# Kernel optimization log

Hardware: AMD Instinct MI355X
Metric: run time of the kernel (lower is better)

## Reference

```python
import jax, jax.numpy as jnp
import numpy as np

B, N, NB = 48, 512, 4096
SEG = ((0, 1600), (1600, 3200), (3200, 4096))  # static bond-type segments (C-C, C-H, H-H)
H, L = 8, 2                                     # be MLP hidden width / depth
BOTOL = 0.001
LP1, OVUN3, OVUN4, OVUN6, OVUN7, OVUN8 = 10.0, 5.0, 3.0, 6.0, 1.0, 12.0
BOX = 10.0


def _taper(r, rmin, rmax):
    # piecewise smooth step used on the uncorrected bond-order terms
    r3 = jnp.where(r > rmax, 1.0, 0.0)
    ok = (r <= rmax) & (r > rmin)
    r2 = jnp.where(ok, r, 0.0)
    r20 = jnp.where(ok, 1.0, 0.0)
    rterm = 1.0 / (rmin - rmax) ** 3
    rm = rmin * r20
    rd = rm - r2
    trm1 = rm + 2.0 * r2 - 3.0 * rmax * r20
    return rterm * rd * rd * trm1 + r3


def _div_if(y, x):
    return y / jnp.where(x != 0.0, x, 1e-8)


def setup_inputs():
    key = jax.random.key(0)
    ks = jax.random.split(key, 10)
    x = jax.random.uniform(ks[0], (B, N, 3), dtype=jnp.float32) * BOX
    cell = jnp.eye(3, dtype=jnp.float32) * BOX
    rcell = jnp.eye(3, dtype=jnp.float32) / BOX
    i = jax.random.randint(ks[1], (NB,), 0, N)
    j = jax.random.randint(ks[2], (NB,), 0, N)
    j = jnp.where(i == j, (j + 1) % N, j)
    bdid = jnp.stack([i, j], axis=1).astype(jnp.int32)
    atom_type = jax.random.randint(ks[3], (N,), 0, 2).astype(jnp.int32)
    # per-bond-type ReaxFF parameters (realistic magnitudes)
    bond_rosi = jnp.array([1.38, 1.12, 0.74], jnp.float32)
    bond_bo1 = jnp.array([-0.075, -0.05, -0.08], jnp.float32)
    bond_bo2 = jnp.array([6.8, 6.9, 6.0], jnp.float32)
    bond_ropi = jnp.array([1.28, 1.00, 0.70], jnp.float32)
    bond_bo3 = jnp.array([-0.20, -0.15, -0.20], jnp.float32)
    bond_bo4 = jnp.array([8.5, 7.0, 8.0], jnp.float32)
    bond_ropp = jnp.array([1.20, 0.90, 0.65], jnp.float32)
    bond_bo5 = jnp.array([-0.30, -0.25, -0.30], jnp.float32)
    bond_bo6 = jnp.array([10.0, 9.0, 10.0], jnp.float32)
    bond_Desi = jnp.array([145.0, 180.0, 160.0], jnp.float32)
    # per-species parameters (C, H)
    sp_val = jnp.array([4.0, 1.0], jnp.float32)
    sp_vale = jnp.array([4.0, 1.0], jnp.float32)
    sp_lp2 = jnp.array([0.1, 0.0], jnp.float32)
    sp_ovun2 = jnp.array([-5.0, -10.0], jnp.float32)
    sp_ovun5 = jnp.array([30.0, 0.0], jnp.float32)
    # fe (bond-energy) MLP weights per bond type: Wi (3,H), Wh (H,H)xL, Wo (H,1)
    fe_wi = jax.random.normal(ks[4], (3, 3, H), jnp.float32) * 0.5
    fe_w = jax.random.normal(ks[5], (3, L, H, H), jnp.float32) * 0.5
    fe_b = jax.random.normal(ks[6], (3, L, H), jnp.float32) * 0.5
    fe_wo = jax.random.normal(ks[7], (3, H, 1), jnp.float32) * 0.5
    fe_bo = jax.random.normal(ks[8], (3, 1), jnp.float32) * 0.5
    return dict(x=x, cell=cell, rcell=rcell, bdid=bdid, atom_type=atom_type,
                bond_rosi=bond_rosi, bond_bo1=bond_bo1, bond_bo2=bond_bo2,
                bond_ropi=bond_ropi, bond_bo3=bond_bo3, bond_bo4=bond_bo4,
                bond_ropp=bond_ropp, bond_bo5=bond_bo5, bond_bo6=bond_bo6,
                bond_Desi=bond_Desi, sp_val=sp_val, sp_vale=sp_vale,
                sp_lp2=sp_lp2, sp_ovun2=sp_ovun2, sp_ovun5=sp_ovun5,
                fe_wi=fe_wi, fe_w=fe_w, fe_b=fe_b, fe_wo=fe_wo, fe_bo=fe_bo)


def _forward(x, cell, rcell, bdid, atom_type,
             bond_rosi, bond_bo1, bond_bo2, bond_ropi, bond_bo3, bond_bo4,
             bond_ropp, bond_bo5, bond_bo6, bond_Desi,
             sp_val, sp_vale, sp_lp2, sp_ovun2, sp_ovun5,
             fe_wi, fe_w, fe_b, fe_wo, fe_bo):
    # --- all-pairs distances with minimum-image wrapping (fvr + rcell/cell) ---
    vr = x[:, :, None, :] - x[:, None, :, :]              # [B,N,N,3]
    vrf = vr @ rcell
    vrf = jnp.where(vrf - 0.5 > 0, vrf - 1.0, vrf)
    vrf = jnp.where(vrf + 0.5 < 0, vrf + 1.0, vrf)
    vr = vrf @ cell
    r = jnp.sqrt(jnp.sum(vr * vr, axis=3))                # [B,N,N]
    ii, jj = bdid[:, 0], bdid[:, 1]
    rbd_all = r[:, ii, jj]                                # [B,NB]

    si_l, pi_l, pp_l, ebd_l = [], [], [], []
    for t, (s0, s1) in enumerate(SEG):
        rbd = rbd_all[:, s0:s1]
        # uncorrected bond orders (get_bondorder_uc)
        eterm1 = (1.0 + BOTOL) * jnp.exp(bond_bo1[t] * (rbd / bond_rosi[t]) ** bond_bo2[t])
        eterm2 = jnp.exp(bond_bo3[t] * (rbd / bond_ropi[t]) ** bond_bo4[t])
        eterm3 = jnp.exp(bond_bo5[t] * (rbd / bond_ropp[t]) ** bond_bo6[t])
        bosi = _taper(eterm1, BOTOL, 2.0 * BOTOL) * (eterm1 - BOTOL)
        bopi = _taper(eterm2, BOTOL, 2.0 * BOTOL) * eterm2
        bopp = _taper(eterm3, BOTOL, 2.0 * BOTOL) * eterm3
        # bond-energy sigmoid MLP (fnn 'fe'): input [bosi,bopi,bopp]
        X = jnp.stack([bosi, bopi, bopp], axis=-1)        # [B,nb_t,3]
        h = jax.nn.sigmoid(jnp.einsum('bni,ih->bnh', X, fe_wi[t]))
        for l in range(L):
            h = jax.nn.sigmoid(h @ fe_w[t, l] + fe_b[t, l])
        esi = jax.nn.sigmoid(h @ fe_wo[t] + fe_bo[t])[..., 0]
        ebd_l.append(-bond_Desi[t] * esi)
        si_l.append(bosi); pi_l.append(bopi); pp_l.append(bopp)

    bosi = jnp.concatenate(si_l, axis=1)
    bopi = jnp.concatenate(pi_l, axis=1)
    bopp = jnp.concatenate(pp_l, axis=1)
    ebond = jnp.sum(jnp.concatenate(ebd_l, axis=1), axis=1)   # [B]

    # per-atom coordination via symmetric scatter of bond orders
    bo = bosi + bopi + bopp
    bpi = bopi + bopp
    zeros = jnp.zeros((x.shape[0], x.shape[1]), x.dtype)
    Delta = zeros.at[:, ii].add(bo).at[:, jj].add(bo)
    Delta_pi = zeros.at[:, ii].add(bpi).at[:, jj].add(bpi)
    SO = zeros.at[:, ii].add(bosi).at[:, jj].add(bosi)

    # species-indexed gathers of atomic params (self.s[st][sp] boolean gathers)
    val = sp_val[atom_type][None, :]
    vale = sp_vale[atom_type][None, :]
    lp2 = sp_lp2[atom_type][None, :]
    ovun2 = sp_ovun2[atom_type][None, :]
    ovun5 = sp_ovun5[atom_type][None, :]

    # --- elone ---
    Nlp = 0.5 * (vale - val)
    delta_e = 0.5 * (Delta - vale)
    De = -jax.nn.relu(-jnp.ceil(delta_e))
    nlp = -De + jnp.exp(-LP1 * 4.0 * jnp.square(1.0 + delta_e - De))
    Delta_lp = jax.nn.relu(Nlp - nlp + 1.0) - 1.0
    Elone = lp2 * Delta_lp / (1.0 + jnp.exp(-75.0 * Delta_lp))

    # --- eover ---
    delta_lpcorr = Delta - val - Delta_lp / (1.0 + OVUN3 * jnp.exp(OVUN4 * Delta_pi))
    otrm1 = _div_if(1.0, delta_lpcorr + val)
    Eover = SO * otrm1 * delta_lpcorr * jax.nn.sigmoid(-ovun2 * delta_lpcorr)

    # --- eunder ---
    expeu1 = jnp.exp(OVUN6 * delta_lpcorr)
    eu1 = jax.nn.sigmoid(ovun2 * delta_lpcorr)
    eu2 = 1.0 / (1.0 + OVUN7 * jnp.exp(OVUN8 * Delta_pi))
    Eunder = -ovun5 * (1.0 - expeu1) * eu1 * eu2

    return ebond + jnp.sum(Elone + Eover + Eunder, axis=1)   # [B]


def reference(x, cell, rcell, bdid, atom_type,
              bond_rosi, bond_bo1, bond_bo2, bond_ropi, bond_bo3, bond_bo4,
              bond_ropp, bond_bo5, bond_bo6, bond_Desi,
              sp_val, sp_vale, sp_lp2, sp_ovun2, sp_ovun5,
              fe_wi, fe_w, fe_b, fe_wo, fe_bo):
    return _forward(x, cell, rcell, bdid, atom_type,
                    bond_rosi, bond_bo1, bond_bo2, bond_ropi, bond_bo3, bond_bo4,
                    bond_ropp, bond_bo5, bond_bo6, bond_Desi,
                    sp_val, sp_vale, sp_lp2, sp_ovun2, sp_ovun5,
                    fe_wi, fe_w, fe_b, fe_wo, fe_bo)
```

## Files before the change

### kernel.cpp

```cpp
#include <hip/hip_runtime.h>
#include <math.h>

#define B_    48
#define N_    512
#define NBOND 4096
#define H_    8
#define L_    2
#define G_    16
#define TPB1  256
#define BPB   (NBOND / G_)
#define TPB2  512

#define LOG2E 1.44269504f

__device__ __forceinline__ float rcpf(float x)  { return __builtin_amdgcn_rcpf(x); }
__device__ __forceinline__ float exp2g(float x) { return __builtin_amdgcn_exp2f(x); }
__device__ __forceinline__ float log2g(float x) { return __builtin_amdgcn_logf(x); }
__device__ __forceinline__ float expg(float x)  { return exp2g(x * LOG2E); }
__device__ __forceinline__ float sigf(float x)  { return rcpf(1.0f + expg(-x)); }

__device__ __forceinline__ float taperf(float r) {
    const float rmin = 0.001f, rmax = 0.002f;
    const float d = rmin - rmax;
    const float rterm = 1.0f / (d * d * d);
    float r3  = (r > rmax) ? 1.0f : 0.0f;
    bool ok   = (r <= rmax) && (r > rmin);
    float r2  = ok ? r : 0.0f;
    float r20 = ok ? 1.0f : 0.0f;
    float rm   = rmin * r20;
    float rd   = rm - r2;
    float trm1 = rm + 2.0f * r2 - 3.0f * rmax * r20;
    return rterm * rd * rd * trm1 + r3;
}

#define WI_OFF   0
#define W_OFF    72
#define BV_OFF   456
#define WO_OFF   504
#define BO_OFF   528
#define WTOT     531

__global__ __launch_bounds__(TPB1) void bond_kernel(
    const float* __restrict__ x, const float* __restrict__ cell, const float* __restrict__ rcell,
    const int*  __restrict__ bdid,
    const float* __restrict__ rosi, const float* __restrict__ bo1, const float* __restrict__ bo2,
    const float* __restrict__ ropi, const float* __restrict__ bo3, const float* __restrict__ bo4,
    const float* __restrict__ ropp, const float* __restrict__ bo5, const float* __restrict__ bo6,
    const float* __restrict__ Desi,
    const float* __restrict__ wi, const float* __restrict__ w, const float* __restrict__ bvec,
    const float* __restrict__ wo, const float* __restrict__ bo_out,
    float* __restrict__ pPart, float* __restrict__ pEbd)
{
    const int b   = blockIdx.x / G_;
    const int g   = blockIdx.x % G_;
    const int tid = threadIdx.x;

    __shared__ float sS[N_], sP[N_];
    __shared__ float sw[WTOT];
    __shared__ float sder[30];
    __shared__ float swave[TPB1 / 64];

    #pragma unroll
    for (int q = tid; q < N_; q += TPB1) { sS[q] = 0.0f; sP[q] = 0.0f; }
    for (int q = tid; q < WTOT; q += TPB1) {
        float v;
        if      (q < W_OFF)  v = wi[q - WI_OFF];
        else if (q < BV_OFF) v = w[q - W_OFF];
        else if (q < WO_OFF) v = bvec[q - BV_OFF];
        else if (q < BO_OFF) v = wo[q - WO_OFF];
        else                 v = bo_out[q - BO_OFF];
        sw[q] = v;
    }
    if (tid < 3) {
        sder[tid * 10 + 0] = log2g(rosi[tid]);
        sder[tid * 10 + 1] = log2g(ropi[tid]);
        sder[tid * 10 + 2] = log2g(ropp[tid]);
        sder[tid * 10 + 3] = bo1[tid] * LOG2E;
        sder[tid * 10 + 4] = bo3[tid] * LOG2E;
        sder[tid * 10 + 5] = bo5[tid] * LOG2E;
        sder[tid * 10 + 6] = bo2[tid];
        sder[tid * 10 + 7] = bo4[tid];
        sder[tid * 10 + 8] = bo6[tid];
        sder[tid * 10 + 9] = Desi[tid];
    }
    float c00 = cell[0], c01 = cell[1], c02 = cell[2];
    float c10 = cell[3], c11 = cell[4], c12 = cell[5];
    float c20 = cell[6], c21 = cell[7], c22 = cell[8];
    float q00 = rcell[0], q01 = rcell[1], q02 = rcell[2];
    float q10 = rcell[3], q11 = rcell[4], q12 = rcell[5];
    float q20 = rcell[6], q21 = rcell[7], q22 = rcell[8];
    __syncthreads();

    const float* xb = x + (size_t)b * (N_ * 3);

    int k = g * BPB + tid;
    int t = (k < 1600) ? 0 : ((k < 3200) ? 1 : 2);
    const float* dc = sder + t * 10;

    int2 ij = ((const int2*)bdid)[k];
    int i = ij.x, j = ij.y;

    float vx = xb[3 * i + 0] - xb[3 * j + 0];
    float vy = xb[3 * i + 1] - xb[3 * j + 1];
    float vz = xb[3 * i + 2] - xb[3 * j + 2];

    float f0 = vx * q00 + vy * q10 + vz * q20;
    float f1 = vx * q01 + vy * q11 + vz * q21;
    float f2 = vx * q02 + vy * q12 + vz * q22;
    f0 = (f0 - 0.5f > 0.0f) ? f0 - 1.0f : f0;  f0 = (f0 + 0.5f < 0.0f) ? f0 + 1.0f : f0;
    f1 = (f1 - 0.5f > 0.0f) ? f1 - 1.0f : f1;  f1 = (f1 + 0.5f < 0.0f) ? f1 + 1.0f : f1;
    f2 = (f2 - 0.5f > 0.0f) ? f2 - 1.0f : f2;  f2 = (f2 + 0.5f < 0.0f) ? f2 + 1.0f : f2;
    float wx = f0 * c00 + f1 * c10 + f2 * c20;
    float wy = f0 * c01 + f1 * c11 + f2 * c21;
    float wz = f0 * c02 + f1 * c12 + f2 * c22;
    float r = __builtin_amdgcn_sqrtf(wx * wx + wy * wy + wz * wz);

    float lr = log2g(r);
    float p1 = exp2g(dc[6] * (lr - dc[0]));
    float p2 = exp2g(dc[7] * (lr - dc[1]));
    float p3 = exp2g(dc[8] * (lr - dc[2]));
    float e1 = 1.001f * exp2g(dc[3] * p1);
    float e2 = exp2g(dc[4] * p2);
    float e3 = exp2g(dc[5] * p3);
    float bosi = taperf(e1) * (e1 - 0.001f);
    float bopi = taperf(e2) * e2;
    float bopp = taperf(e3) * e3;

    const float* Wi = sw + WI_OFF + t * 24;
    const float* Wm = sw + W_OFF  + t * (L_ * H_ * H_);
    const float* Bv = sw + BV_OFF + t * (L_ * H_);
    const float* Wo = sw + WO_OFF + t * H_;
    float h[H_], h2[H_];
    #pragma unroll
    for (int hh = 0; hh < H_; ++hh) {
        float s = bosi * Wi[0 * H_ + hh] + bopi * Wi[1 * H_ + hh] + bopp * Wi[2 * H_ + hh];
        h[hh] = sigf(s);
    }
    #pragma unroll
    for (int l = 0; l < L_; ++l) {
        #pragma unroll
        for (int ho = 0; ho < H_; ++ho) {
            float s = Bv[l * H_ + ho];
            #pragma unroll
            for (int hi = 0; hi < H_; ++hi)
                s += h[hi] * Wm[l * (H_ * H_) + hi * H_ + ho];
            h2[ho] = sigf(s);
        }
        #pragma unroll
        for (int hh = 0; hh < H_; ++hh) h[hh] = h2[hh];
    }
    float o = sw[BO_OFF + t];
    #pragma unroll
    for (int hi = 0; hi < H_; ++hi) o += h[hi] * Wo[hi];
    float ebd = -dc[9] * sigf(o);

    float bpi = bopi + bopp;
    atomicAdd(&sS[i], bosi); atomicAdd(&sS[j], bosi);
    atomicAdd(&sP[i], bpi);  atomicAdd(&sP[j], bpi);
    __syncthreads();

    float* pd = pPart + (size_t)(b * G_ + g) * (2 * N_);
    #pragma unroll
    for (int q = tid; q < N_; q += TPB1) {
        pd[q]      = sS[q];
        pd[N_ + q] = sP[q];
    }

    float v = ebd;
    for (int off = 32; off > 0; off >>= 1) v += __shfl_down(v, off, 64);
    int lane = tid & 63, wid = tid >> 6;
    if (lane == 0) swave[wid] = v;
    __syncthreads();
    if (tid == 0) {
        float s = 0.0f;
        #pragma unroll
        for (int wv = 0; wv < TPB1 / 64; ++wv) s += swave[wv];
        pEbd[b * G_ + g] = s;
    }
}

__global__ __launch_bounds__(TPB2) void atom_kernel(
    const int* __restrict__ atype,
    const float* __restrict__ sval, const float* __restrict__ svale, const float* __restrict__ slp2,
    const float* __restrict__ sov2, const float* __restrict__ sov5,
    const float* __restrict__ pPart, const float* __restrict__ pEbd,
    float* __restrict__ out)
{
    const int b   = blockIdx.x;
    const int tid = threadIdx.x;
    __shared__ float swave[TPB2 / 64];

    float so = 0.0f, DP = 0.0f;
    #pragma unroll
    for (int g = 0; g < G_; ++g) {
        const float* pd = pPart + (size_t)(b * G_ + g) * (2 * N_);
        so += pd[tid];
        DP += pd[N_ + tid];
    }
    float D = so + DP;

    int at = atype[tid];
    float val  = sval[at];
    float vale = svale[at];
    float lp2  = slp2[at];
    float ov2  = sov2[at];
    float ov5  = sov5[at];

    float Nlp = 0.5f * (vale - val);
    float de  = 0.5f * (D - vale);
    float De  = fminf(ceilf(de), 0.0f);
    float t1  = 1.0f + de - De;
    float nlp = -De + expg(-40.0f * t1 * t1);
    float Dlp = fmaxf(Nlp - nlp + 1.0f, 0.0f) - 1.0f;
    float Elone = lp2 * Dlp * rcpf(1.0f + expg(-75.0f * Dlp));

    float dlc = D - val - Dlp * rcpf(1.0f + 5.0f * expg(3.0f * DP));
    float denom = dlc + val;
    float ot = rcpf((denom != 0.0f) ? denom : 1e-8f);
    float Eover = so * ot * dlc * sigf(-ov2 * dlc);

    float expeu1 = expg(6.0f * dlc);
    float eu1 = sigf(ov2 * dlc);
    float eu2 = rcpf(1.0f + expg(12.0f * DP));
    float Eunder = -ov5 * (1.0f - expeu1) * eu1 * eu2;

    float e = Elone + Eover + Eunder;
    if (tid < G_) e += pEbd[b * G_ + tid];

    float v = e;
    for (int off = 32; off > 0; off >>= 1) v += __shfl_down(v, off, 64);
    int lane = tid & 63, wid = tid >> 6;
    if (lane == 0) swave[wid] = v;
    __syncthreads();
    if (tid == 0) {
        float s = 0.0f;
        #pragma unroll
        for (int wv = 0; wv < TPB2 / 64; ++wv) s += swave[wv];
        out[b] = s;
    }
}

extern "C" void kernel_launch(void* const* d_in, const int* in_sizes, int n_in,
                              void* d_out, int out_size, void* d_ws, size_t ws_size,
                              hipStream_t stream)
{
    const float* x     = (const float*)d_in[0];
    const float* cell  = (const float*)d_in[1];
    const float* rcell = (const float*)d_in[2];
    const int*   bdid  = (const int*)d_in[3];
    const int*   atype = (const int*)d_in[4];
    const float* rosi  = (const float*)d_in[5];
    const float* bo1   = (const float*)d_in[6];
    const float* bo2   = (const float*)d_in[7];
    const float* ropi  = (const float*)d_in[8];
    const float* bo3   = (const float*)d_in[9];
    const float* bo4   = (const float*)d_in[10];
    const float* ropp  = (const float*)d_in[11];
    const float* bo5   = (const float*)d_in[12];
    const float* bo6   = (const float*)d_in[13];
    const float* Desi  = (const float*)d_in[14];
    const float* sval  = (const float*)d_in[15];
    const float* svale = (const float*)d_in[16];
    const float* slp2  = (const float*)d_in[17];
    const float* sov2  = (const float*)d_in[18];
    const float* sov5  = (const float*)d_in[19];
    const float* wi    = (const float*)d_in[20];
    const float* w     = (const float*)d_in[21];
    const float* bvec  = (const float*)d_in[22];
    const float* wo    = (const float*)d_in[23];
    const float* bo_o  = (const float*)d_in[24];
    float* out = (float*)d_out;

    float* pPart = (float*)d_ws;
    float* pEbd  = pPart + (size_t)B_ * G_ * 2 * N_;

    bond_kernel<<<B_ * G_, TPB1, 0, stream>>>(
        x, cell, rcell, bdid,
        rosi, bo1, bo2, ropi, bo3, bo4, ropp, bo5, bo6, Desi,
        wi, w, bvec, wo, bo_o,
        pPart, pEbd);

    atom_kernel<<<B_, TPB2, 0, stream>>>(
        atype, sval, svale, slp2, sov2, sov5,
        pPart, pEbd, out);
}
```

Before: 17.72 us.

## Load MLP weights via wave-uniform scalar reads and drop block reduction syncs

The bond kernel no longer stages MLP weights and per-type constants into shared memory. It reads them straight from global memory with a wave-uniform type index taken by readfirstlane, so they can be fetched as scalar loads. That removes the staging loop and the barrier before compute, and the one remaining barrier moves to just before the shared atomics. Per-block partial sums are now written as interleaved float2 pairs, and the per-wave energy sums go straight to the workspace, so the final block-level reduction and its barrier are gone. The scheme relies on the bond-type segment boundaries lining up with 64-wide wavefronts, and the atom kernel now reads four times as many energy partials.

```diff
diff --git a/kernel.cpp b/kernel.cpp
--- a/kernel.cpp
+++ b/kernel.cpp
@@ -10,6 +10,7 @@
 #define TPB1  256
 #define BPB   (NBOND / G_)
 #define TPB2  512
+#define NW1   (TPB1 / 64)
 
 #define LOG2E 1.44269504f
 
@@ -33,13 +34,6 @@
     return rterm * rd * rd * trm1 + r3;
 }
 
-#define WI_OFF   0
-#define W_OFF    72
-#define BV_OFF   456
-#define WO_OFF   504
-#define BO_OFF   528
-#define WTOT     531
-
 __global__ __launch_bounds__(TPB1) void bond_kernel(
     const float* __restrict__ x, const float* __restrict__ cell, const float* __restrict__ rcell,
     const int*  __restrict__ bdid,
@@ -49,53 +43,38 @@
     const float* __restrict__ Desi,
     const float* __restrict__ wi, const float* __restrict__ w, const float* __restrict__ bvec,
     const float* __restrict__ wo, const float* __restrict__ bo_out,
-    float* __restrict__ pPart, float* __restrict__ pEbd)
+    float2* __restrict__ pPart, float* __restrict__ pEbd)
 {
     const int b   = blockIdx.x / G_;
     const int g   = blockIdx.x % G_;
     const int tid = threadIdx.x;
 
     __shared__ float sS[N_], sP[N_];
-    __shared__ float sw[WTOT];
-    __shared__ float sder[30];
-    __shared__ float swave[TPB1 / 64];
-
-    #pragma unroll
-    for (int q = tid; q < N_; q += TPB1) { sS[q] = 0.0f; sP[q] = 0.0f; }
-    for (int q = tid; q < WTOT; q += TPB1) {
-        float v;
-        if      (q < W_OFF)  v = wi[q - WI_OFF];
-        else if (q < BV_OFF) v = w[q - W_OFF];
-        else if (q < WO_OFF) v = bvec[q - BV_OFF];
-        else if (q < BO_OFF) v = wo[q - WO_OFF];
-        else                 v = bo_out[q - BO_OFF];
-        sw[q] = v;
-    }
-    if (tid < 3) {
-        sder[tid * 10 + 0] = log2g(rosi[tid]);
-        sder[tid * 10 + 1] = log2g(ropi[tid]);
-        sder[tid * 10 + 2] = log2g(ropp[tid]);
-        sder[tid * 10 + 3] = bo1[tid] * LOG2E;
-        sder[tid * 10 + 4] = bo3[tid] * LOG2E;
-        sder[tid * 10 + 5] = bo5[tid] * LOG2E;
-        sder[tid * 10 + 6] = bo2[tid];
-        sder[tid * 10 + 7] = bo4[tid];
-        sder[tid * 10 + 8] = bo6[tid];
-        sder[tid * 10 + 9] = Desi[tid];
-    }
+
+    sS[tid] = 0.0f;        sP[tid] = 0.0f;
+    sS[tid + TPB1] = 0.0f; sP[tid + TPB1] = 0.0f;
+
     float c00 = cell[0], c01 = cell[1], c02 = cell[2];
     float c10 = cell[3], c11 = cell[4], c12 = cell[5];
     float c20 = cell[6], c21 = cell[7], c22 = cell[8];
     float q00 = rcell[0], q01 = rcell[1], q02 = rcell[2];
     float q10 = rcell[3], q11 = rcell[4], q12 = rcell[5];
     float q20 = rcell[6], q21 = rcell[7], q22 = rcell[8];
-    __syncthreads();
 
     const float* xb = x + (size_t)b * (N_ * 3);
 
     int k = g * BPB + tid;
     int t = (k < 1600) ? 0 : ((k < 3200) ? 1 : 2);
-    const float* dc = sder + t * 10;
+    const int ts = __builtin_amdgcn_readfirstlane(t);
+
+    float lro_si = log2g(rosi[ts]);
+    float lro_pi = log2g(ropi[ts]);
+    float lro_pp = log2g(ropp[ts]);
+    float cb1 = bo1[ts] * LOG2E;
+    float cb3 = bo3[ts] * LOG2E;
+    float cb5 = bo5[ts] * LOG2E;
+    float pw2 = bo2[ts], pw4 = bo4[ts], pw6 = bo6[ts];
+    float des = Desi[ts];
 
     int2 ij = ((const int2*)bdid)[k];
     int i = ij.x, j = ij.y;
@@ -116,20 +95,21 @@
     float r = __builtin_amdgcn_sqrtf(wx * wx + wy * wy + wz * wz);
 
     float lr = log2g(r);
-    float p1 = exp2g(dc[6] * (lr - dc[0]));
-    float p2 = exp2g(dc[7] * (lr - dc[1]));
-    float p3 = exp2g(dc[8] * (lr - dc[2]));
-    float e1 = 1.001f * exp2g(dc[3] * p1);
-    float e2 = exp2g(dc[4] * p2);
-    float e3 = exp2g(dc[5] * p3);
+    float p1 = exp2g(pw2 * (lr - lro_si));
+    float p2 = exp2g(pw4 * (lr - lro_pi));
+    float p3 = exp2g(pw6 * (lr - lro_pp));
+    float e1 = 1.001f * exp2g(cb1 * p1);
+    float e2 = exp2g(cb3 * p2);
+    float e3 = exp2g(cb5 * p3);
     float bosi = taperf(e1) * (e1 - 0.001f);
     float bopi = taperf(e2) * e2;
     float bopp = taperf(e3) * e3;
 
-    const float* Wi = sw + WI_OFF + t * 24;
-    const float* Wm = sw + W_OFF  + t * (L_ * H_ * H_);
-    const float* Bv = sw + BV_OFF + t * (L_ * H_);
-    const float* Wo = sw + WO_OFF + t * H_;
+    const float* Wi = wi + ts * 24;
+    const float* Wm = w + ts * (L_ * H_ * H_);
+    const float* Bv = bvec + ts * (L_ * H_);
+    const float* Wo = wo + ts * H_;
+
     float h[H_], h2[H_];
     #pragma unroll
     for (int hh = 0; hh < H_; ++hh) {
@@ -149,41 +129,32 @@
         #pragma unroll
         for (int hh = 0; hh < H_; ++hh) h[hh] = h2[hh];
     }
-    float o = sw[BO_OFF + t];
+    float o = bo_out[ts];
     #pragma unroll
     for (int hi = 0; hi < H_; ++hi) o += h[hi] * Wo[hi];
-    float ebd = -dc[9] * sigf(o);
+    float ebd = -des * sigf(o);
 
     float bpi = bopi + bopp;
+    __syncthreads();
     atomicAdd(&sS[i], bosi); atomicAdd(&sS[j], bosi);
     atomicAdd(&sP[i], bpi);  atomicAdd(&sP[j], bpi);
     __syncthreads();
 
-    float* pd = pPart + (size_t)(b * G_ + g) * (2 * N_);
-    #pragma unroll
-    for (int q = tid; q < N_; q += TPB1) {
-        pd[q]      = sS[q];
-        pd[N_ + q] = sP[q];
-    }
+    float2* pd = pPart + (size_t)(b * G_ + g) * N_;
+    pd[tid]        = make_float2(sS[tid],        sP[tid]);
+    pd[tid + TPB1] = make_float2(sS[tid + TPB1], sP[tid + TPB1]);
 
     float v = ebd;
     for (int off = 32; off > 0; off >>= 1) v += __shfl_down(v, off, 64);
     int lane = tid & 63, wid = tid >> 6;
-    if (lane == 0) swave[wid] = v;
-    __syncthreads();
-    if (tid == 0) {
-        float s = 0.0f;
-        #pragma unroll
-        for (int wv = 0; wv < TPB1 / 64; ++wv) s += swave[wv];
-        pEbd[b * G_ + g] = s;
-    }
+    if (lane == 0) pEbd[(b * G_ + g) * NW1 + wid] = v;
 }
 
 __global__ __launch_bounds__(TPB2) void atom_kernel(
     const int* __restrict__ atype,
     const float* __restrict__ sval, const float* __restrict__ svale, const float* __restrict__ slp2,
     const float* __restrict__ sov2, const float* __restrict__ sov5,
-    const float* __restrict__ pPart, const float* __restrict__ pEbd,
+    const float2* __restrict__ pPart, const float* __restrict__ pEbd,
     float* __restrict__ out)
 {
     const int b   = blockIdx.x;
@@ -193,9 +164,9 @@
     float so = 0.0f, DP = 0.0f;
     #pragma unroll
     for (int g = 0; g < G_; ++g) {
-        const float* pd = pPart + (size_t)(b * G_ + g) * (2 * N_);
-        so += pd[tid];
-        DP += pd[N_ + tid];
+        float2 v = pPart[(size_t)(b * G_ + g) * N_ + tid];
+        so += v.x;
+        DP += v.y;
     }
     float D = so + DP;
 
@@ -225,7 +196,7 @@
     float Eunder = -ov5 * (1.0f - expeu1) * eu1 * eu2;
 
     float e = Elone + Eover + Eunder;
-    if (tid < G_) e += pEbd[b * G_ + tid];
+    if (tid < G_ * NW1) e += pEbd[b * (G_ * NW1) + tid];
 
     float v = e;
     for (int off = 32; off > 0; off >>= 1) v += __shfl_down(v, off, 64);
@@ -271,8 +242,8 @@
     const float* bo_o  = (const float*)d_in[24];
     float* out = (float*)d_out;
 
-    float* pPart = (float*)d_ws;
-    float* pEbd  = pPart + (size_t)B_ * G_ * 2 * N_;
+    float2* pPart = (float2*)d_ws;
+    float*  pEbd  = (float*)(pPart + (size_t)B_ * G_ * N_);
 
     bond_kernel<<<B_ * G_, TPB1, 0, stream>>>(
         x, cell, rcell, bdid,
```

After: 16.30 us. 8.0% less time.
